# Kernel tuning notes

Hardware: AMD Instinct MI355X
Metric: run time of the kernel (lower is better)

## Reference

```python
import jax, jax.numpy as jnp
import numpy as np


def _conv(x, w, stride, padding):
    # x: [N, Cin, H, W], w: [Cout, Cin, kh, kw]
    return jax.lax.conv_general_dilated(
        x, w, window_strides=(stride, stride), padding=padding,
        dimension_numbers=("NCHW", "OIHW", "NCHW"))


def _reflect_pad1(x):
    return jnp.pad(x, ((0, 0), (0, 0), (1, 1), (1, 1)), mode="reflect")


def setup_inputs() -> dict:
    key = jax.random.key(0)
    k1, k2, k3, k4 = jax.random.split(key, 4)
    B, C, H, W = 16, 3, 512, 512
    NC = 20  # num_channels (intermediate width)
    # xavier-uniform-like scales
    x = jax.random.normal(k1, (B, C, H, W), dtype=jnp.float32)
    w1 = jax.random.normal(k2, (NC, 1, 4, 4), dtype=jnp.float32) * (6.0 / (1 * 16 + NC * 16)) ** 0.5
    w2 = jax.random.normal(k3, (NC, NC, 4, 4), dtype=jnp.float32) * (6.0 / (NC * 16 + NC * 16)) ** 0.5
    w3 = jax.random.normal(k4, (1, NC, 3, 3), dtype=jnp.float32) * (6.0 / (NC * 9 + 1 * 9)) ** 0.5
    return {"x": x, "w1": w1, "w2": w2, "w3": w3}


def reference(x, w1, w2, w3):
    # Original torch code loops over input channels; equivalently fold the
    # channel dim into the batch dim and run the whole pipeline once.
    B, C, H, W = x.shape
    xr = x.reshape(B * C, 1, H, W)
    # stage 1: reflect pad 1 + 4x4 stride-2 conv + relu
    o1 = jax.nn.relu(_conv(_reflect_pad1(xr), w1, 2, "VALID"))  # [B*C, NC, 256, 256]
    # stage 2: reflect pad 1 + 4x4 stride-2 conv + relu
    o2 = jax.nn.relu(_conv(_reflect_pad1(o1), w2, 2, "VALID"))  # [B*C, NC, 128, 128]
    # stage 3: 3x3 conv, zero padding 1, + relu -> 1 channel per input channel
    o3 = jax.nn.relu(_conv(o2, w3, 1, ((1, 1), (1, 1))))        # [B*C, 1, 128, 128]
    Ho, Wo = o3.shape[-2], o3.shape[-1]
    return o3.reshape(B, C, Ho, Wo)
```

## Files before the change

kernel.cpp:

```cpp
#include <hip/hip_runtime.h>


#define NC 20
#define TS 12
#define S1RP 600
#define S1CIN 30
#define SO2 14
#define PS2 196
#define NWG (48 * 121)
#define CPX (NWG / 8)

#define W2F_OFF 256
#define W3_OFF  5376
#define WP_N    5556

typedef _Float16 h2  __attribute__((ext_vector_type(2)));
typedef __fp16   hq2 __attribute__((ext_vector_type(2)));
typedef _Float16 h8  __attribute__((ext_vector_type(8)));
typedef float    f32x16 __attribute__((ext_vector_type(16)));

__device__ __forceinline__ float dot2(unsigned int a, unsigned int b, float c) {
    return __builtin_amdgcn_fdot2(__builtin_bit_cast(h2, a),
                                  __builtin_bit_cast(h2, b), c, false);
}
__device__ __forceinline__ unsigned int packh(float a, float b) {
    _Float16 ha = (_Float16)a, hb = (_Float16)b;
    return (unsigned int)__builtin_bit_cast(unsigned short, ha) |
           ((unsigned int)__builtin_bit_cast(unsigned short, hb) << 16);
}
__device__ __forceinline__ unsigned int pkrtz(float a, float b) {
    hq2 r = __builtin_amdgcn_cvt_pkrtz(a, b);
    return __builtin_bit_cast(unsigned int, r);
}
__device__ __forceinline__ unsigned int pk_relu(unsigned int u) {
    unsigned int r;
    asm("v_pk_max_f16 %0, %1, 0" : "=v"(r) : "v"(u));
    return r;
}
__device__ __forceinline__ int refl256(int q) {
    q = (q < 0) ? -q : q; return (q > 255) ? 510 - q : q;
}
__device__ __forceinline__ int refl512(int q) {
    q = (q < 0) ? -q : q; return (q > 511) ? 1022 - q : q;
}

__global__ __launch_bounds__(256) void pack_weights(
    const float* __restrict__ w1, const float* __restrict__ w2,
    const float* __restrict__ w3, unsigned int* __restrict__ wp)
{
    const int i = blockIdx.x * 256 + threadIdx.x;
    if (i >= WP_N) return;
    if (i < W2F_OFF) {
        const int lane = i >> 2, jp = i & 3;
        const int ch = lane & 31, k0 = (lane >> 5) * 8 + 2 * jp;
        wp[i] = (ch < NC) ? packh(w1[ch * 16 + k0], w1[ch * 16 + k0 + 1]) : 0u;
    } else if (i < W3_OFF) {
        const int t = i - W2F_OFF;
        const int cin = t >> 8, r = t & 255;
        const int lane = r >> 2, jp = r & 3;
        const int cout = lane & 31;
        const int k0 = (lane >> 5) * 8 + ((jp & 1) << 2) + ((jp >> 1) << 1);
        wp[i] = (cout < NC) ? packh(w2[(cout * NC + cin) * 16 + k0],
                                    w2[(cout * NC + cin) * 16 + k0 + 1]) : 0u;
    } else {
        const int t = i - W3_OFF;
        const int c = t / 9;
        const int r = t - c * 9;
        const int di = r / 3, wh = r - di * 3;
        const float* row = w3 + c * 9 + di * 3;
        float a, b;
        if (wh == 0)      { a = row[0]; b = row[1]; }
        else if (wh == 1) { a = row[2]; b = 0.f;    }
        else              { a = 0.f;    b = row[2]; }
        wp[i] = packh(a, b);
    }
}

__device__ __forceinline__ void load_taps(
    const float* __restrict__ xi, int t0, int h, int wv, int kh,
    bool rowEdge, bool colEdge, int vb, int v0, int v1, int v2, int v3,
    unsigned int xw[4][4])
{
    #pragma unroll
    for (int i = 0; i < 4; ++i) {
        const int c = wv + 4 * i;
        const int t = t0 + 14 * h + c;
        int rlo, rhi;
        if (!rowEdge) {
            rlo = 2 * t - 3 + 2 * kh;
            rhi = rlo + 1;
        } else {
            const int mr = refl256(t - 1);
            const int rb = 2 * mr - 1 + 2 * kh;
            rlo = refl512(rb);
            rhi = refl512(rb + 1);
        }
        const float* __restrict__ plo = xi + rlo * 512;
        const float* __restrict__ phi = xi + rhi * 512;
        float f0, f1, f2, f3, f4, f5, f6, f7;
        if (!colEdge) {
            f0 = plo[vb]; f1 = plo[vb + 1]; f2 = plo[vb + 2]; f3 = plo[vb + 3];
            f4 = phi[vb]; f5 = phi[vb + 1]; f6 = phi[vb + 2]; f7 = phi[vb + 3];
        } else {
            f0 = plo[v0]; f1 = plo[v1]; f2 = plo[v2]; f3 = plo[v3];
            f4 = phi[v0]; f5 = phi[v1]; f6 = phi[v2]; f7 = phi[v3];
        }
        xw[i][0] = pkrtz(f0, f1); xw[i][1] = pkrtz(f2, f3);
        xw[i][2] = pkrtz(f4, f5); xw[i][3] = pkrtz(f6, f7);
    }
}

__global__ __launch_bounds__(256, 3) void ds_fused(
    const float* __restrict__ x,
    const unsigned int* __restrict__ wp,
    float* __restrict__ out)
{
    __shared__ __attribute__((aligned(16))) unsigned short s_o1[15 * S1RP * 2];
    __shared__ __attribute__((aligned(16))) unsigned short s_o2[NC * PS2];

    const int rawb = blockIdx.x;
    const int bid  = (rawb & 7) * CPX + (rawb >> 3);

    const int img  = bid / 121;
    const int t121 = bid - img * 121;
    const int ty   = t121 / 11;
    const int tx   = t121 - ty * 11;
    const int y0   = ty * TS;
    const int x0   = tx * TS;
    const int tid  = threadIdx.x;
    const int lane = tid & 63;
    const int wv   = tid >> 6;
    const int l31  = lane & 31;
    const int kh   = lane >> 5;

    const float* __restrict__ xi = x + (size_t)img * (512 * 512);
    const uint4* __restrict__ w1f = (const uint4*)wp;
    const uint4* __restrict__ w2f = (const uint4*)(wp + W2F_OFF);
    const unsigned int* __restrict__ w3p = wp + W3_OFF;

    const int t0 = 2 * y0 - 2;
    const int s0 = 2 * x0 - 2;

    const int sA = s0 + l31;
    const bool rowEdge = (ty == 0) || (ty == 10);
    const bool colEdge = (tx == 0) || (tx == 10);
    const bool interior = !rowEdge && !colEdge;
    const int vb = 2 * sA - 3;
    int v0 = 0, v1 = 0, v2 = 0, v3 = 0;
    if (colEdge) {
        const int n2 = refl256(sA - 1);
        const int vbb = 2 * n2 - 1;
        v0 = refl512(vbb);     v1 = refl512(vbb + 1);
        v2 = refl512(vbb + 2); v3 = refl512(vbb + 3);
    }
    const h8 w1frag = __builtin_bit_cast(h8, w1f[lane]);

    const int q  = 32 * wv + l31;
    const int qc = (q < 98) ? q : 0;
    const int li = (qc * 2341) >> 15;
    const int jl = qc - li * 14;
    const int offR0 = (li + kh) * (S1RP / 2) + jl;
    const int offR1 = offR0 + 7 * (S1RP / 2);

    unsigned int* const s1d = (unsigned int*)s_o1;
    const uint2* const so1v = (const uint2*)s_o1;

    unsigned int xw0[4][4], xw1[4][4];
    load_taps(xi, t0, 0, wv, kh, rowEdge, colEdge, vb, v0, v1, v2, v3, xw0);
    load_taps(xi, t0, 1, wv, kh, rowEdge, colEdge, vb, v0, v1, v2, v3, xw1);

    uint4 bwr[NC];
    #pragma unroll
    for (int cin = 0; cin < NC; ++cin) bwr[cin] = w2f[cin * 64 + lane];

    #pragma unroll
    for (int i = 0; i < 4; ++i) {
        const int c = wv + 4 * i;
        uint4 aw; aw.x = xw0[i][0]; aw.y = xw0[i][1];
                  aw.z = xw0[i][2]; aw.w = xw0[i][3];
        f32x16 o = {};
        o = __builtin_amdgcn_mfma_f32_32x32x16_f16(
                __builtin_bit_cast(h8, aw), w1frag, o, 0, 0, 0);
        if (l31 < NC) {
            unsigned int* wr = s1d + (c >> 1) * S1RP + l31 * S1CIN + (c & 1);
            const int kb = 4 * kh;
            wr[kb + 0]  = pk_relu(pkrtz(o[0],  o[1]));
            wr[kb + 2]  = pk_relu(pkrtz(o[2],  o[3]));
            wr[kb + 8]  = pk_relu(pkrtz(o[4],  o[5]));
            wr[kb + 10] = pk_relu(pkrtz(o[6],  o[7]));
            wr[kb + 16] = pk_relu(pkrtz(o[8],  o[9]));
            wr[kb + 18] = pk_relu(pkrtz(o[10], o[11]));
            wr[kb + 24] = pk_relu(pkrtz(o[12], o[13]));
            if (kh == 0)
                wr[kb + 26] = pk_relu(pkrtz(o[14], o[15]));
        }
    }
    #pragma unroll
    for (int i = 0; i < 4; ++i) {
        const int c = wv + 4 * i;
        uint4 aw; aw.x = xw1[i][0]; aw.y = xw1[i][1];
                  aw.z = xw1[i][2]; aw.w = xw1[i][3];
        f32x16 o = {};
        o = __builtin_amdgcn_mfma_f32_32x32x16_f16(
                __builtin_bit_cast(h8, aw), w1frag, o, 0, 0, 0);
        if (l31 < NC && c >= 2) {
            unsigned int* wr =
                s1d + (7 + (c >> 1)) * S1RP + l31 * S1CIN + (c & 1);
            const int kb = 4 * kh;
            wr[kb + 0]  = pk_relu(pkrtz(o[0],  o[1]));
            wr[kb + 2]  = pk_relu(pkrtz(o[2],  o[3]));
            wr[kb + 8]  = pk_relu(pkrtz(o[4],  o[5]));
            wr[kb + 10] = pk_relu(pkrtz(o[6],  o[7]));
            wr[kb + 16] = pk_relu(pkrtz(o[8],  o[9]));
            wr[kb + 18] = pk_relu(pkrtz(o[10], o[11]));
            wr[kb + 24] = pk_relu(pkrtz(o[12], o[13]));
            if (kh == 0)
                wr[kb + 26] = pk_relu(pkrtz(o[14], o[15]));
        }
    }
    __syncthreads();

    f32x16 acc0 = {}, acc1 = {};
    #pragma unroll
    for (int cin = 0; cin < NC; ++cin) {
        const uint2* pA0 = so1v + cin * (S1CIN / 2) + offR0;
        const uint2* pA1 = so1v + cin * (S1CIN / 2) + offR1;
        const uint2 lo0 = pA0[0], hi0 = pA0[1];
        const uint2 lo1 = pA1[0], hi1 = pA1[1];
        uint4 aw0; aw0.x = lo0.x; aw0.y = lo0.y; aw0.z = hi0.x; aw0.w = hi0.y;
        uint4 aw1; aw1.x = lo1.x; aw1.y = lo1.y; aw1.z = hi1.x; aw1.w = hi1.y;
        acc0 = __builtin_amdgcn_mfma_f32_32x32x16_f16(
                   __builtin_bit_cast(h8, aw0),
                   __builtin_bit_cast(h8, bwr[cin]), acc0, 0, 0, 0);
        acc1 = __builtin_amdgcn_mfma_f32_32x32x16_f16(
                   __builtin_bit_cast(h8, aw1),
                   __builtin_bit_cast(h8, bwr[cin]), acc1, 0, 0, 0);
    }

    if (l31 < NC) {
        #pragma unroll
        for (int h = 0; h < 2; ++h) {
            const f32x16& acc = h ? acc1 : acc0;
            unsigned short* bp = &s_o2[l31 * PS2 + 98 * h + 32 * wv + 4 * kh];
            if (interior) {
                #pragma unroll
                for (int j = 0; j < 4; ++j) {
                    const int Q = 32 * wv + 4 * kh + 8 * j;
                    if (Q < 98)
                        *(unsigned int*)(bp + 8 * j) =
                            pk_relu(pkrtz(acc[4 * j], acc[4 * j + 1]));
                    if (Q + 2 < 98)
                        *(unsigned int*)(bp + 8 * j + 2) =
                            pk_relu(pkrtz(acc[4 * j + 2], acc[4 * j + 3]));
                }
            } else {
                #pragma unroll
                for (int d = 0; d < 8; ++d) {
                    const int jj = d >> 1, ss = d & 1;
                    const int Qd = 32 * wv + 4 * kh + 8 * jj + 2 * ss;
                    if (Qd < 98) {
                        const int li2 = (Qd * 2341) >> 15;
                        const int jl2 = Qd - li2 * 14;
                        const int oi  = y0 - 1 + 7 * h + li2;
                        const int oj  = x0 - 1 + jl2;
                        const bool rok = (oi >= 0) && (oi < 128);
                        const unsigned int m =
                            (rok && oj >= 0 && oj < 128 ? 0x0000FFFFu : 0u) |
                            (rok && oj + 1 < 128        ? 0xFFFF0000u : 0u);
                        *(unsigned int*)(bp + 8 * jj + 2 * ss) =
                            pk_relu(pkrtz(acc[4 * jj + 2 * ss],
                                          acc[4 * jj + 2 * ss + 1])) & m;
                    }
                }
            }
        }
    }
    __syncthreads();

    if (tid < TS * TS) {
        const int oy = tid / TS;
        const int ox = tid - oy * TS;
        const int e  = ox & ~1;
        const int par = ox & 1;
        const unsigned int shp = (unsigned int)(par << 4);
        const unsigned int* wsel = w3p + 1 + par;
        float a0 = 0.f, a1 = 0.f, a2 = 0.f;
        #pragma unroll
        for (int c = 0; c < NC; ++c) {
            const unsigned short* pl = &s_o2[c * PS2 + oy * SO2 + e];
            #pragma unroll
            for (int di = 0; di < 3; ++di) {
                const unsigned int* row = (const unsigned int*)(pl + di * SO2);
                const unsigned int d0 = row[0];
                const unsigned int d1 = row[1];
                const unsigned int u0 = __builtin_amdgcn_alignbit(d1, d0, shp);
                const unsigned int wa = w3p[c * 9 + di * 3 + 0];
                const unsigned int wz = wsel[c * 9 + di * 3];
                float& aR = (di == 0) ? a0 : ((di == 1) ? a1 : a2);
                aR = dot2(u0, wa, aR);
                aR = dot2(d1, wz, aR);
            }
        }
        const float accc = a0 + a1 + a2;
        const int gy = y0 + oy, gx = x0 + ox;
        if (gy < 128 && gx < 128)
            out[(size_t)img * (128 * 128) + gy * 128 + gx] = fmaxf(accc, 0.f);
    }
}

extern "C" void kernel_launch(void* const* d_in, const int* in_sizes, int n_in,
                              void* d_out, int out_size, void* d_ws, size_t ws_size,
                              hipStream_t stream) {
    const float* x  = (const float*)d_in[0];
    const float* w1 = (const float*)d_in[1];
    const float* w2 = (const float*)d_in[2];
    const float* w3 = (const float*)d_in[3];
    unsigned int* wp = (unsigned int*)d_ws;
    float* out = (float*)d_out;
    pack_weights<<<dim3((WP_N + 255) / 256), dim3(256), 0, stream>>>(w1, w2, w3, wp);
    ds_fused<<<dim3(NWG), dim3(256), 0, stream>>>(x, wp, out);
}
```

Baseline: 155.4 us.

## Process two images per workgroup and prefetch next image's input taps

```diff
diff --git a/kernel.cpp b/kernel.cpp
--- a/kernel.cpp
+++ b/kernel.cpp
@@ -7,7 +7,7 @@
 #define S1CIN 30
 #define SO2 14
 #define PS2 196
-#define NWG (48 * 121)
+#define NWG (24 * 121)
 #define CPX (NWG / 8)
 
 #define W2F_OFF 256
@@ -110,69 +110,10 @@
     }
 }
 
-__global__ __launch_bounds__(256, 3) void ds_fused(
-    const float* __restrict__ x,
-    const unsigned int* __restrict__ wp,
-    float* __restrict__ out)
-{
-    __shared__ __attribute__((aligned(16))) unsigned short s_o1[15 * S1RP * 2];
-    __shared__ __attribute__((aligned(16))) unsigned short s_o2[NC * PS2];
-
-    const int rawb = blockIdx.x;
-    const int bid  = (rawb & 7) * CPX + (rawb >> 3);
-
-    const int img  = bid / 121;
-    const int t121 = bid - img * 121;
-    const int ty   = t121 / 11;
-    const int tx   = t121 - ty * 11;
-    const int y0   = ty * TS;
-    const int x0   = tx * TS;
-    const int tid  = threadIdx.x;
-    const int lane = tid & 63;
-    const int wv   = tid >> 6;
-    const int l31  = lane & 31;
-    const int kh   = lane >> 5;
-
-    const float* __restrict__ xi = x + (size_t)img * (512 * 512);
-    const uint4* __restrict__ w1f = (const uint4*)wp;
-    const uint4* __restrict__ w2f = (const uint4*)(wp + W2F_OFF);
-    const unsigned int* __restrict__ w3p = wp + W3_OFF;
-
-    const int t0 = 2 * y0 - 2;
-    const int s0 = 2 * x0 - 2;
-
-    const int sA = s0 + l31;
-    const bool rowEdge = (ty == 0) || (ty == 10);
-    const bool colEdge = (tx == 0) || (tx == 10);
-    const bool interior = !rowEdge && !colEdge;
-    const int vb = 2 * sA - 3;
-    int v0 = 0, v1 = 0, v2 = 0, v3 = 0;
-    if (colEdge) {
-        const int n2 = refl256(sA - 1);
-        const int vbb = 2 * n2 - 1;
-        v0 = refl512(vbb);     v1 = refl512(vbb + 1);
-        v2 = refl512(vbb + 2); v3 = refl512(vbb + 3);
-    }
-    const h8 w1frag = __builtin_bit_cast(h8, w1f[lane]);
-
-    const int q  = 32 * wv + l31;
-    const int qc = (q < 98) ? q : 0;
-    const int li = (qc * 2341) >> 15;
-    const int jl = qc - li * 14;
-    const int offR0 = (li + kh) * (S1RP / 2) + jl;
-    const int offR1 = offR0 + 7 * (S1RP / 2);
-
-    unsigned int* const s1d = (unsigned int*)s_o1;
-    const uint2* const so1v = (const uint2*)s_o1;
-
-    unsigned int xw0[4][4], xw1[4][4];
-    load_taps(xi, t0, 0, wv, kh, rowEdge, colEdge, vb, v0, v1, v2, v3, xw0);
-    load_taps(xi, t0, 1, wv, kh, rowEdge, colEdge, vb, v0, v1, v2, v3, xw1);
-
-    uint4 bwr[NC];
-    #pragma unroll
-    for (int cin = 0; cin < NC; ++cin) bwr[cin] = w2f[cin * 64 + lane];
-
+__device__ __forceinline__ void stage_a(
+    const unsigned int xw0[4][4], const unsigned int xw1[4][4],
+    unsigned int* s1d, const h8& w1frag, int wv, int l31, int kh)
+{
     #pragma unroll
     for (int i = 0; i < 4; ++i) {
         const int c = wv + 4 * i;
@@ -218,9 +159,12 @@
                 wr[kb + 26] = pk_relu(pkrtz(o[14], o[15]));
         }
     }
-    __syncthreads();
-
-    f32x16 acc0 = {}, acc1 = {};
+}
+
+__device__ __forceinline__ void stage_b(
+    const uint2* so1v, const uint4 bwr[NC], int offR0, int offR1,
+    f32x16& acc0, f32x16& acc1)
+{
     #pragma unroll
     for (int cin = 0; cin < NC; ++cin) {
         const uint2* pA0 = so1v + cin * (S1CIN / 2) + offR0;
@@ -236,45 +180,132 @@
                    __builtin_bit_cast(h8, aw1),
                    __builtin_bit_cast(h8, bwr[cin]), acc1, 0, 0, 0);
     }
-
-    if (l31 < NC) {
-        #pragma unroll
-        for (int h = 0; h < 2; ++h) {
-            const f32x16& acc = h ? acc1 : acc0;
-            unsigned short* bp = &s_o2[l31 * PS2 + 98 * h + 32 * wv + 4 * kh];
-            if (interior) {
-                #pragma unroll
-                for (int j = 0; j < 4; ++j) {
-                    const int Q = 32 * wv + 4 * kh + 8 * j;
-                    if (Q < 98)
-                        *(unsigned int*)(bp + 8 * j) =
-                            pk_relu(pkrtz(acc[4 * j], acc[4 * j + 1]));
-                    if (Q + 2 < 98)
-                        *(unsigned int*)(bp + 8 * j + 2) =
-                            pk_relu(pkrtz(acc[4 * j + 2], acc[4 * j + 3]));
-                }
-            } else {
-                #pragma unroll
-                for (int d = 0; d < 8; ++d) {
-                    const int jj = d >> 1, ss = d & 1;
-                    const int Qd = 32 * wv + 4 * kh + 8 * jj + 2 * ss;
-                    if (Qd < 98) {
-                        const int li2 = (Qd * 2341) >> 15;
-                        const int jl2 = Qd - li2 * 14;
-                        const int oi  = y0 - 1 + 7 * h + li2;
-                        const int oj  = x0 - 1 + jl2;
-                        const bool rok = (oi >= 0) && (oi < 128);
-                        const unsigned int m =
-                            (rok && oj >= 0 && oj < 128 ? 0x0000FFFFu : 0u) |
-                            (rok && oj + 1 < 128        ? 0xFFFF0000u : 0u);
-                        *(unsigned int*)(bp + 8 * jj + 2 * ss) =
-                            pk_relu(pkrtz(acc[4 * jj + 2 * ss],
-                                          acc[4 * jj + 2 * ss + 1])) & m;
-                    }
+}
+
+__device__ __forceinline__ void epilogue(
+    const f32x16& acc0, const f32x16& acc1, unsigned short* s2p,
+    int l31, int wv, int kh, bool interior, int y0, int x0)
+{
+    if (l31 >= NC) return;
+    #pragma unroll
+    for (int h = 0; h < 2; ++h) {
+        const f32x16& acc = h ? acc1 : acc0;
+        unsigned short* bp = &s2p[l31 * PS2 + 98 * h + 32 * wv + 4 * kh];
+        if (interior) {
+            #pragma unroll
+            for (int j = 0; j < 4; ++j) {
+                const int Q = 32 * wv + 4 * kh + 8 * j;
+                if (Q < 98)
+                    *(unsigned int*)(bp + 8 * j) =
+                        pk_relu(pkrtz(acc[4 * j], acc[4 * j + 1]));
+                if (Q + 2 < 98)
+                    *(unsigned int*)(bp + 8 * j + 2) =
+                        pk_relu(pkrtz(acc[4 * j + 2], acc[4 * j + 3]));
+            }
+        } else {
+            #pragma unroll
+            for (int d = 0; d < 8; ++d) {
+                const int jj = d >> 1, ss = d & 1;
+                const int Qd = 32 * wv + 4 * kh + 8 * jj + 2 * ss;
+                if (Qd < 98) {
+                    const int li2 = (Qd * 2341) >> 15;
+                    const int jl2 = Qd - li2 * 14;
+                    const int oi  = y0 - 1 + 7 * h + li2;
+                    const int oj  = x0 - 1 + jl2;
+                    const bool rok = (oi >= 0) && (oi < 128);
+                    const unsigned int m =
+                        (rok && oj >= 0 && oj < 128 ? 0x0000FFFFu : 0u) |
+                        (rok && oj + 1 < 128        ? 0xFFFF0000u : 0u);
+                    *(unsigned int*)(bp + 8 * jj + 2 * ss) =
+                        pk_relu(pkrtz(acc[4 * jj + 2 * ss],
+                                      acc[4 * jj + 2 * ss + 1])) & m;
                 }
             }
         }
     }
+}
+
+__global__ __launch_bounds__(256, 3) void ds_fused(
+    const float* __restrict__ x,
+    const unsigned int* __restrict__ wp,
+    float* __restrict__ out)
+{
+    __shared__ __attribute__((aligned(16))) unsigned short s_o1[15 * S1RP * 2];
+    __shared__ __attribute__((aligned(16))) unsigned short s_o2[2 * NC * PS2];
+
+    const int rawb = blockIdx.x;
+    const int bid  = (rawb & 7) * CPX + (rawb >> 3);
+
+    const int pair = bid / 121;
+    const int t121 = bid - pair * 121;
+    const int ty   = t121 / 11;
+    const int tx   = t121 - ty * 11;
+    const int y0   = ty * TS;
+    const int x0   = tx * TS;
+    const int tid  = threadIdx.x;
+    const int lane = tid & 63;
+    const int wv   = tid >> 6;
+    const int l31  = lane & 31;
+    const int kh   = lane >> 5;
+
+    const float* __restrict__ xi0 = x + (size_t)(2 * pair) * (512 * 512);
+    const float* __restrict__ xi1 = xi0 + 512 * 512;
+    const uint4* __restrict__ w1f = (const uint4*)wp;
+    const uint4* __restrict__ w2f = (const uint4*)(wp + W2F_OFF);
+    const unsigned int* __restrict__ w3p = wp + W3_OFF;
+
+    const int t0 = 2 * y0 - 2;
+    const int s0 = 2 * x0 - 2;
+
+    const int sA = s0 + l31;
+    const bool rowEdge = (ty == 0) || (ty == 10);
+    const bool colEdge = (tx == 0) || (tx == 10);
+    const bool interior = !rowEdge && !colEdge;
+    const int vb = 2 * sA - 3;
+    int v0 = 0, v1 = 0, v2 = 0, v3 = 0;
+    if (colEdge) {
+        const int n2 = refl256(sA - 1);
+        const int vbb = 2 * n2 - 1;
+        v0 = refl512(vbb);     v1 = refl512(vbb + 1);
+        v2 = refl512(vbb + 2); v3 = refl512(vbb + 3);
+    }
+    const h8 w1frag = __builtin_bit_cast(h8, w1f[lane]);
+
+    const int q  = 32 * wv + l31;
+    const int qc = (q < 98) ? q : 0;
+    const int li = (qc * 2341) >> 15;
+    const int jl = qc - li * 14;
+    const int offR0 = (li + kh) * (S1RP / 2) + jl;
+    const int offR1 = offR0 + 7 * (S1RP / 2);
+
+    unsigned int* const s1d = (unsigned int*)s_o1;
+    const uint2* const so1v = (const uint2*)s_o1;
+
+    unsigned int xwA[4][4], xwB[4][4], xwC[4][4];
+    load_taps(xi0, t0, 0, wv, kh, rowEdge, colEdge, vb, v0, v1, v2, v3, xwA);
+    load_taps(xi0, t0, 1, wv, kh, rowEdge, colEdge, vb, v0, v1, v2, v3, xwB);
+    load_taps(xi1, t0, 0, wv, kh, rowEdge, colEdge, vb, v0, v1, v2, v3, xwC);
+    uint4 bwr[NC];
+    #pragma unroll
+    for (int cin = 0; cin < NC; ++cin) bwr[cin] = w2f[cin * 64 + lane];
+
+    stage_a(xwA, xwB, s1d, w1frag, wv, l31, kh);
+    __syncthreads();
+
+    f32x16 acc0 = {}, acc1 = {};
+    stage_b(so1v, bwr, offR0, offR1, acc0, acc1);
+    epilogue(acc0, acc1, s_o2, l31, wv, kh, interior, y0, x0);
+    __syncthreads();
+
+    unsigned int xwD[4][4];
+    load_taps(xi1, t0, 1, wv, kh, rowEdge, colEdge, vb, v0, v1, v2, v3, xwD);
+
+    stage_a(xwC, xwD, s1d, w1frag, wv, l31, kh);
+    __syncthreads();
+
+    f32x16 acc2 = {}, acc3 = {};
+    stage_b(so1v, bwr, offR0, offR1, acc2, acc3);
+    epilogue(acc2, acc3, s_o2 + NC * PS2, l31, wv, kh, interior, y0, x0);
     __syncthreads();
 
     if (tid < TS * TS) {
@@ -284,27 +315,35 @@
         const int par = ox & 1;
         const unsigned int shp = (unsigned int)(par << 4);
         const unsigned int* wsel = w3p + 1 + par;
-        float a0 = 0.f, a1 = 0.f, a2 = 0.f;
+        const int gy = y0 + oy, gx = x0 + ox;
+        const bool gok = (gy < 128) && (gx < 128);
         #pragma unroll
-        for (int c = 0; c < NC; ++c) {
-            const unsigned short* pl = &s_o2[c * PS2 + oy * SO2 + e];
+        for (int cw = 0; cw < 2; ++cw) {
+            const unsigned short* s2b = s_o2 + cw * (NC * PS2);
+            float a0 = 0.f, a1 = 0.f, a2 = 0.f;
             #pragma unroll
-            for (int di = 0; di < 3; ++di) {
-                const unsigned int* row = (const unsigned int*)(pl + di * SO2);
-                const unsigned int d0 = row[0];
-                const unsigned int d1 = row[1];
-                const unsigned int u0 = __builtin_amdgcn_alignbit(d1, d0, shp);
-                const unsigned int wa = w3p[c * 9 + di * 3 + 0];
-                const unsigned int wz = wsel[c * 9 + di * 3];
-                float& aR = (di == 0) ? a0 : ((di == 1) ? a1 : a2);
-                aR = dot2(u0, wa, aR);
-                aR = dot2(d1, wz, aR);
+            for (int c = 0; c < NC; ++c) {
+                const unsigned short* pl = &s2b[c * PS2 + oy * SO2 + e];
+                #pragma unroll
+                for (int di = 0; di < 3; ++di) {
+                    const unsigned int* row =
+                        (const unsigned int*)(pl + di * SO2);
+                    const unsigned int d0 = row[0];
+                    const unsigned int d1 = row[1];
+                    const unsigned int u0 =
+                        __builtin_amdgcn_alignbit(d1, d0, shp);
+                    const unsigned int wa = w3p[c * 9 + di * 3 + 0];
+                    const unsigned int wz = wsel[c * 9 + di * 3];
+                    float& aR = (di == 0) ? a0 : ((di == 1) ? a1 : a2);
+                    aR = dot2(u0, wa, aR);
+                    aR = dot2(d1, wz, aR);
+                }
             }
-        }
-        const float accc = a0 + a1 + a2;
-        const int gy = y0 + oy, gx = x0 + ox;
-        if (gy < 128 && gx < 128)
-            out[(size_t)img * (128 * 128) + gy * 128 + gx] = fmaxf(accc, 0.f);
+            const float accc = a0 + a1 + a2;
+            if (gok)
+                out[(size_t)(2 * pair + cw) * (128 * 128) + gy * 128 + gx] =
+                    fmaxf(accc, 0.f);
+        }
     }
 }
 
```

New measurement: 218.9 us. 1.41x slower.
